# Optimization experiments

Measured on AMD Instinct MI355X. Metric: run time of the kernel, lower is better.

Reference implementation:

```python
import jax, jax.numpy as jnp
import numpy as np
from jax import lax

B, L, H, E, NIN, D = 1024, 128, 256, 256, 3, 10


def setup_inputs():
    key = jax.random.key(0)
    ks = jax.random.split(key, 32)
    s = 0.05

    def rn(i, shape):
        return jax.random.normal(ks[i], shape, dtype=jnp.float32) * s

    inp = {
        "received": jax.random.normal(ks[0], (B, L, NIN), dtype=jnp.float32),
        "encoder_hidden": jax.random.normal(ks[1], (B, L, E), dtype=jnp.float32),
        "h0": jax.random.normal(ks[2], (2, B, H), dtype=jnp.float32),
    }
    i = 3
    for r in (1, 2):
        for l, din in ((0, NIN), (1, H)):
            inp[f"w_ih{r}_l{l}"] = rn(i, (3 * H, din)); i += 1
            inp[f"w_hh{r}_l{l}"] = rn(i, (3 * H, H)); i += 1
            inp[f"b_ih{r}_l{l}"] = rn(i, (3 * H,)); i += 1
            inp[f"b_hh{r}_l{l}"] = rn(i, (3 * H,)); i += 1
    inp["attn_W"] = rn(i, (H, H + E)); i += 1
    inp["v_W"] = rn(i, (1, H)); i += 1
    inp["out_W"] = rn(i, (1, 2 * (H + E))); i += 1
    inp["out_b"] = rn(i, (1,))
    return inp


def _gru_cell(x, h, w_ih, w_hh, b_ih, b_hh):
    # PyTorch GRU cell semantics (gate order r, z, n)
    gi = x @ w_ih.T + b_ih
    gh = h @ w_hh.T + b_hh
    i_r, i_z, i_n = jnp.split(gi, 3, axis=-1)
    h_r, h_z, h_n = jnp.split(gh, 3, axis=-1)
    r = jax.nn.sigmoid(i_r + h_r)
    z = jax.nn.sigmoid(i_z + h_z)
    n = jnp.tanh(i_n + r * h_n)
    return (1.0 - z) * n + z * h


def _forward(received, encoder_hidden, h0, p1, p2, attn_W, v_W, out_W, out_b):
    # split attn weight: cat order is (s, encoder_hidden)
    W_s, W_e = attn_W[:, :H], attn_W[:, H:]
    # precompute encoder part of the attention energy once
    attn_enc = jnp.einsum('bse,he->bsh', encoder_hidden, W_e)  # [B,L,H]
    v = v_W[0]

    def attend(s_top):  # s_top: [B,H] = second-layer hidden BEFORE the RNN step
        energy = jnp.tanh((s_top @ W_s.T)[:, None, :] + attn_enc)  # [B,L,H]
        a = jax.nn.softmax(jnp.einsum('bsh,h->bs', energy, v), axis=1)
        return jnp.einsum('bs,bse->be', a, encoder_hidden)  # context [B,E]

    def rnn2(x, h, p):  # 2-layer GRU, single timestep
        h0n = _gru_cell(x, h[0], p[0], p[1], p[2], p[3])
        h1n = _gru_cell(h0n, h[1], p[4], p[5], p[6], p[7])
        return jnp.stack([h0n, h1n]), h1n

    def step(carry, x_t):
        h1, h2 = carry
        c1 = attend(h1[1])
        c2 = attend(h2[1])
        h1n, o1 = rnn2(x_t, h1, p1)
        h2n, o2 = rnn2(x_t, h2, p2)
        return (h1n, h2n), (jnp.concatenate([o1, c1], -1), jnp.concatenate([o2, c2], -1))

    xs = jnp.swapaxes(received, 0, 1)  # [L,B,NIN]
    _, (r1, r2) = lax.scan(step, (h0, h0), xs)
    rnn_out1 = jnp.swapaxes(r1, 0, 1)  # [B,L,H+E]
    rnn_out2 = jnp.swapaxes(r2, 0, 1)

    # delayed second stream: index i+D, clamped to L-1 for i >= L-D-1
    t = jnp.arange(L)
    idx = jnp.where(t >= L - D - 1, L - 1, t + D)
    rnn_out = jnp.concatenate([rnn_out1, rnn_out2[:, idx, :]], axis=-1)  # [B,L,2*(H+E)]
    return jax.nn.sigmoid(rnn_out @ out_W.T + out_b)  # [B,L,1]


def reference(received, encoder_hidden, h0,
              w_ih1_l0, w_hh1_l0, b_ih1_l0, b_hh1_l0,
              w_ih1_l1, w_hh1_l1, b_ih1_l1, b_hh1_l1,
              w_ih2_l0, w_hh2_l0, b_ih2_l0, b_hh2_l0,
              w_ih2_l1, w_hh2_l1, b_ih2_l1, b_hh2_l1,
              attn_W, v_W, out_W, out_b):
    p1 = (w_ih1_l0, w_hh1_l0, b_ih1_l0, b_hh1_l0, w_ih1_l1, w_hh1_l1, b_ih1_l1, b_hh1_l1)
    p2 = (w_ih2_l0, w_hh2_l0, b_ih2_l0, b_hh2_l0, w_ih2_l1, w_hh2_l1, b_ih2_l1, b_hh2_l1)
    return _forward(received, encoder_hidden, h0, p1, p2, attn_W, v_W, out_W, out_b)
```

## Files before the change

kernel.cpp:

```cpp
#include <hip/hip_runtime.h>

typedef unsigned int u32;
typedef unsigned short u16;
typedef __attribute__((ext_vector_type(8))) short bf8v;
typedef __attribute__((ext_vector_type(4))) float f32x4;

#define NB 1024
#define NL 128
#define NH 256

#define WS_WHH(g,l)  ((size_t)((g)*2+(l)) * 393216ull)
#define WS_WIHX(g)   (1572864ull + (size_t)(g)*49152ull)
#define WS_WIH1(g)   (1671168ull + (size_t)(g)*442368ull)
#define WS_WSPK      2555904ull
#define WS_WEPK      2686976ull
#define WS_AE        2818048ull
#define WS_HTOP      (WS_AE + 134217728ull)
#define WS_HL0       (WS_HTOP + 135266304ull)
#define WS_P         (WS_HL0 + 134217728ull)
#define WS_Q         (WS_P + 1048576ull)

struct Ins { const float* p[23]; };

__device__ __forceinline__ u16 f2b(float f) {
  u32 u = __builtin_bit_cast(u32, f);
  u += 0x7fffu + ((u >> 16) & 1u);
  return (u16)(u >> 16);
}
__device__ __forceinline__ float b2f(u16 h) { return __builtin_bit_cast(float, ((u32)h) << 16); }
__device__ __forceinline__ float upk(const uint4& q, int i) {
  u32 w = (i < 2) ? q.x : (i < 4) ? q.y : (i < 6) ? q.z : q.w;
  return (i & 1) ? __builtin_bit_cast(float, w & 0xffff0000u)
                 : __builtin_bit_cast(float, w << 16);
}
__device__ __forceinline__ float frcp(float x) { return __builtin_amdgcn_rcpf(x); }
__device__ __forceinline__ float sigm(float x)  { return frcp(1.f + __expf(-x)); }
__device__ __forceinline__ float tanh_f(float x){ return 1.f - 2.f*frcp(1.f + __expf(2.f*x)); }

__device__ __forceinline__ f32x4 MF(bf8v a, bf8v b, f32x4 c) {
  return __builtin_amdgcn_mfma_f32_16x16x32_bf16(a, b, c, 0, 0, 0);
}
__device__ __forceinline__ bf8v ld8(const u16* p) {
  return __builtin_bit_cast(bf8v, *(const uint4*)p);
}

__device__ __forceinline__ void st_h(u16* hout, const u16* hlds, int t, int b0, int tid) {
  int srow = tid >> 5, scol = (tid & 31) * 8;
  *(uint4*)(hout + ((size_t)t*NB + b0 + srow)*NH + scol) = *(const uint4*)(hlds + srow*280 + scol);
}

__global__ void k_pack(Ins in, char* ws) {
  int tile = blockIdx.x*4 + (threadIdx.x >> 6);
  int lane = threadIdx.x & 63, llo = lane & 15, lhi = lane >> 4;
  float v[8];
  u16* dst;
  if (tile < 1536) {
    int mat = tile/384, rem = tile%384, tn = rem >> 3, kt = rem & 7;
    int g = mat >> 1, l = mat & 1;
    const float* w = in.p[4 + g*8 + l*4];
    int n = tn*16 + llo;
    #pragma unroll
    for (int i = 0; i < 8; i++) { int k = kt*32 + lhi*8 + i; v[i] = w[n*256 + k]; }
    dst = (u16*)(ws + WS_WHH(g,l)) + ((size_t)(tn*8+kt)*64 + lane)*8;
  } else if (tile < 1632) {
    int t2 = tile-1536; int g = t2/48, tn = t2%48;
    const float* w  = in.p[3+g*8];
    const float* bi = in.p[5+g*8];
    const float* bh = in.p[6+g*8];
    int n = tn*16 + llo;
    #pragma unroll
    for (int i = 0; i < 8; i++) {
      int k = lhi*8 + i;
      v[i] = (k < 3) ? w[n*3+k] : (k == 3 ? (bi[n] + (n < 512 ? bh[n] : 0.f)) : 0.f);
    }
    dst = (u16*)(ws + WS_WIHX(g)) + ((size_t)tn*64 + lane)*8;
  } else if (tile < 2496) {
    int t2 = tile-1632; int g = t2/432, rem = t2%432, tn = rem/9, kt = rem%9;
    const float* w  = in.p[7+g*8];
    const float* bi = in.p[9+g*8];
    const float* bh = in.p[10+g*8];
    int n = tn*16 + llo;
    #pragma unroll
    for (int i = 0; i < 8; i++) {
      int k = kt*32 + lhi*8 + i;
      v[i] = (k < 256) ? w[n*256+k] : (k == 256 ? (bi[n] + (n < 512 ? bh[n] : 0.f)) : 0.f);
    }
    dst = (u16*)(ws + WS_WIH1(g)) + ((size_t)(tn*9+kt)*64 + lane)*8;
  } else if (tile < 2624) {
    int t2 = tile-2496, tn = t2 >> 3, kt = t2 & 7;
    const float* aw = in.p[19]; int n = tn*16 + llo;
    #pragma unroll
    for (int i = 0; i < 8; i++) { int k = kt*32 + lhi*8 + i; v[i] = aw[n*512 + k]; }
    dst = (u16*)(ws + WS_WSPK) + ((size_t)(tn*8+kt)*64 + lane)*8;
  } else {
    int t2 = tile-2624, tn = t2 >> 3, kt = t2 & 7;
    const float* aw = in.p[19]; int n = tn*16 + llo;
    #pragma unroll
    for (int i = 0; i < 8; i++) { int k = kt*32 + lhi*8 + i; v[i] = aw[n*512 + 256 + k]; }
    dst = (u16*)(ws + WS_WEPK) + ((size_t)(tn*8+kt)*64 + lane)*8;
  }
  uint4 pk;
  pk.x = (u32)f2b(v[0]) | ((u32)f2b(v[1]) << 16);
  pk.y = (u32)f2b(v[2]) | ((u32)f2b(v[3]) << 16);
  pk.z = (u32)f2b(v[4]) | ((u32)f2b(v[5]) << 16);
  pk.w = (u32)f2b(v[6]) | ((u32)f2b(v[7]) << 16);
  *(uint4*)dst = pk;
}

__global__ void k_hall0(Ins in, char* ws) {
  int idx = blockIdx.x*256 + threadIdx.x;
  int g = idx >> 18, r = idx & 262143;
  u16* ht = (u16*)(ws + WS_HTOP) + (size_t)g*(129ull*NB*NH);
  ht[r] = f2b(in.p[2][262144 + r]);
}

__global__ __launch_bounds__(512, 2) void k_attn_enc(Ins in, char* ws) {
  __shared__ __align__(16) u16 alds[128*280];
  const float* eh = in.p[1];
  const u16* wep = (const u16*)(ws + WS_WEPK);
  float* ae = (float*)(ws + WS_AE);
  float* qo = (float*)(ws + WS_Q);
  int b = blockIdx.x, tid = threadIdx.x;
  int w = tid >> 6, lane = tid & 63, llo = lane & 15, lhi = lane >> 4;
  for (int c = tid; c < 4096; c += 512) {
    int row = c >> 5, cc = c & 31;
    const float* s = eh + ((size_t)(b*128 + row))*256 + cc*8;
    float4 f0 = *(const float4*)s, f1 = *(const float4*)(s+4);
    uint4 pk;
    pk.x = (u32)f2b(f0.x) | ((u32)f2b(f0.y) << 16);
    pk.y = (u32)f2b(f0.z) | ((u32)f2b(f0.w) << 16);
    pk.z = (u32)f2b(f1.x) | ((u32)f2b(f1.y) << 16);
    pk.w = (u32)f2b(f1.z) | ((u32)f2b(f1.w) << 16);
    *(uint4*)(alds + row*280 + cc*8) = pk;
  }
  __syncthreads();
  bf8v bf[2][8];
  #pragma unroll
  for (int nt = 0; nt < 2; nt++)
    #pragma unroll
    for (int kt = 0; kt < 8; kt++)
      bf[nt][kt] = ld8(wep + (((size_t)(2*w+nt)*8 + kt)*64 + lane)*8);
  for (int mt = 0; mt < 8; mt++) {
    bf8v af[8];
    #pragma unroll
    for (int kt = 0; kt < 8; kt++)
      af[kt] = ld8(alds + (16*mt + llo)*280 + kt*32 + lhi*8);
    #pragma unroll
    for (int nt = 0; nt < 2; nt++) {
      f32x4 c = {0.f,0.f,0.f,0.f};
      #pragma unroll
      for (int kt = 0; kt < 8; kt++) c = MF(af[kt], bf[nt][kt], c);
      int h = (2*w+nt)*16 + llo;
      int s0 = 16*mt + 4*lhi;
      float4 st = { __expf(2.f*c[0]), __expf(2.f*c[1]), __expf(2.f*c[2]), __expf(2.f*c[3]) };
      *(float4*)(ae + (size_t)b*32768 + h*128 + s0) = st;
    }
  }
  if (tid < 256) {
    int qq = tid >> 7, s = tid & 127;
    const float* wc = in.p[21] + 256 + qq*512;
    float acc = 0.f;
    #pragma unroll 1
    for (int e = 0; e < 256; e += 8) {
      uint4 ev = *(const uint4*)(alds + s*280 + e);
      #pragma unroll
      for (int i = 0; i < 8; i++) acc += upk(ev, i) * wc[e + i];
    }
    qo[((size_t)qq*NB + b)*128 + s] = acc;
  }
}

__global__ __launch_bounds__(512, 2) void k_rec0(Ins in, char* ws) {
  __shared__ __align__(16) u16 hlds[16*280];
  __shared__ __align__(16) u16 xpad[16*32];
  const int g = blockIdx.y, b0 = blockIdx.x*16, tid = threadIdx.x;
  const int w = tid >> 6, lane = tid & 63, llo = lane & 15, lhi = lane >> 4;

  const u16* whh = (const u16*)(ws + WS_WHH(g,0));
  const u16* wgi = (const u16*)(ws + WS_WIHX(g));
  const float* bhh = in.p[6 + g*8];
  const float* h0  = in.p[2];
  const float* recv = in.p[0];
  u16* hout = (u16*)(ws + WS_HL0) + (size_t)g*(128ull*NB*NH);

  float bhhn[2];
  #pragma unroll
  for (int p = 0; p < 2; p++) bhhn[p] = bhh[512 + 32*w + 16*p + llo];

  bf8v whhR[2][8], whhN[2][8];
  #pragma unroll
  for (int p = 0; p < 2; p++)
    #pragma unroll
    for (int kt = 0; kt < 8; kt++) {
      whhR[p][kt] = ld8(whh + (((size_t)(      2*w + p)*8 + kt)*64 + lane)*8);
      whhN[p][kt] = ld8(whh + (((size_t)(32 + 2*w + p)*8 + kt)*64 + lane)*8);
    }

  float hst[2][4];
  #pragma unroll
  for (int r = 0; r < 4; r++) {
    int row = 4*lhi + r;
    #pragma unroll
    for (int p = 0; p < 2; p++) {
      int col = 32*w + 16*p + llo;
      float hv = h0[(size_t)(b0 + row)*NH + col];
      hst[p][r] = hv;
      hlds[row*280 + col] = f2b(hv);
    }
  }
  if (tid < 256) ((u32*)xpad)[tid] = 0u;
  __syncthreads();
  if (tid < 16) {
    const float* x = recv + (size_t)(b0 + tid)*(NL*3);
    uint2 q;
    q.x = (u32)f2b(x[0]) | ((u32)f2b(x[1]) << 16);
    q.y = (u32)f2b(x[2]) | (0x3f80u << 16);
    *(uint2*)(xpad + tid*32) = q;
  }

  #pragma unroll 1
  for (int t = 0; t < NL; t++) {
    __syncthreads();
    if (t) st_h(hout, hlds, t-1, b0, tid);
    bf8v xf = ld8(xpad + llo*32 + lhi*8);
    f32x4 aR[2], aZ[2], aNi[2], aNh[2];
    #pragma unroll
    for (int p = 0; p < 2; p++) {
      f32x4 z = {0.f,0.f,0.f,0.f};
      aR[p]=z; aZ[p]=z; aNi[p]=z; aNh[p]=z;
    }
    #pragma unroll
    for (int q = 0; q < 3; q++)
      #pragma unroll
      for (int p = 0; p < 2; p++) {
        bf8v bt = ld8(wgi + ((size_t)(16*q + 2*w + p)*64 + lane)*8);
        f32x4 a0 = (q==0) ? aR[p] : (q==1) ? aZ[p] : aNi[p];
        a0 = MF(xf, bt, a0);
        if (q==0) aR[p]=a0; else if (q==1) aZ[p]=a0; else aNi[p]=a0;
      }
    #pragma unroll
    for (int kt = 0; kt < 8; kt++) {
      bf8v hf = ld8(hlds + llo*280 + kt*32 + lhi*8);
      #pragma unroll
      for (int p = 0; p < 2; p++) {
        aR[p]  = MF(hf, whhR[p][kt], aR[p]);
        bf8v bz = ld8(whh + (((size_t)(16 + 2*w + p)*8 + kt)*64 + lane)*8);
        aZ[p]  = MF(hf, bz, aZ[p]);
        aNh[p] = MF(hf, whhN[p][kt], aNh[p]);
      }
    }
    u16 hv16[2][4];
    #pragma unroll
    for (int p = 0; p < 2; p++)
      #pragma unroll
      for (int r = 0; r < 4; r++) {
        float rr = sigm(aR[p][r]);
        float zz = sigm(aZ[p][r]);
        float nn = tanh_f(aNi[p][r] + rr*(aNh[p][r] + bhhn[p]));
        float h  = nn + zz*(hst[p][r] - nn);
        hst[p][r] = h; hv16[p][r] = f2b(h);
      }
    __syncthreads();
    #pragma unroll
    for (int r = 0; r < 4; r++) {
      int row = 4*lhi + r;
      #pragma unroll
      for (int p = 0; p < 2; p++)
        hlds[row*280 + 32*w + 16*p + llo] = hv16[p][r];
    }
    if (t < NL-1 && tid < 16) {
      const float* x = recv + (size_t)(b0 + tid)*(NL*3) + (size_t)(t+1)*3;
      uint2 q;
      q.x = (u32)f2b(x[0]) | ((u32)f2b(x[1]) << 16);
      q.y = (u32)f2b(x[2]) | (0x3f80u << 16);
      *(uint2*)(xpad + tid*32) = q;
    }
  }
  __syncthreads();
  st_h(hout, hlds, NL-1, b0, tid);
}

__global__ __launch_bounds__(512, 2) void k_rec1(Ins in, char* ws) {
  __shared__ __align__(16) u16 hlds[16*280];
  __shared__ __align__(16) u16 alds[64*296];
  __shared__ __align__(16) u32 gilds[4*768*9];
  const int g = blockIdx.y, b0 = blockIdx.x*16, tid = threadIdx.x;
  const int w = tid >> 6, lane = tid & 63, llo = lane & 15, lhi = lane >> 4;

  const u16* whh = (const u16*)(ws + WS_WHH(g,1));
  const u16* wgi = (const u16*)(ws + WS_WIH1(g));
  const float* bhh = in.p[10 + g*8];
  const float* h0  = in.p[2] + (size_t)(NB*NH);
  const u16* hl0 = (const u16*)(ws + WS_HL0) + (size_t)g*(128ull*NB*NH);
  u16* hout = (u16*)(ws + WS_HTOP) + (size_t)g*(129ull*NB*NH) + (size_t)(NB*NH);

  float bhhn[2];
  #pragma unroll
  for (int p = 0; p < 2; p++) bhhn[p] = bhh[512 + 32*w + 16*p + llo];

  bf8v whhR[2][8], whhN[2][8];
  #pragma unroll
  for (int p = 0; p < 2; p++)
    #pragma unroll
    for (int kt = 0; kt < 8; kt++) {
      whhR[p][kt] = ld8(whh + (((size_t)(      2*w + p)*8 + kt)*64 + lane)*8);
      whhN[p][kt] = ld8(whh + (((size_t)(32 + 2*w + p)*8 + kt)*64 + lane)*8);
    }

  float hst[2][4];
  #pragma unroll
  for (int r = 0; r < 4; r++) {
    int row = 4*lhi + r;
    #pragma unroll
    for (int p = 0; p < 2; p++) {
      int col = 32*w + 16*p + llo;
      float hv = h0[(size_t)(b0 + row)*NH + col];
      hst[p][r] = hv;
      hlds[row*280 + col] = f2b(hv);
    }
  }

  bf8v af8c = {0,0,0,0,0,0,0,0};
  if (lhi == 0) af8c[0] = (short)0x3f80;

  #pragma unroll 1
  for (int t = 0; t < NL; t++) {
    __syncthreads();
    if (t) st_h(hout, hlds, t-1, b0, tid);
    if ((t & 3) == 0) {
      for (int c = tid; c < 2048; c += 512) {
        int row = c >> 5, cc = c & 31;
        *(uint4*)(alds + row*296 + cc*8) =
          *(const uint4*)(hl0 + ((size_t)(t + (row>>4))*NB + b0 + (row&15))*NH + cc*8);
      }
      __syncthreads();
      #pragma unroll 1
      for (int qq = 0; qq < 3; qq++) {
        f32x4 acc[2][4];
        #pragma unroll
        for (int p = 0; p < 2; p++)
          #pragma unroll
          for (int mt = 0; mt < 4; mt++) { f32x4 z = {0.f,0.f,0.f,0.f}; acc[p][mt] = z; }
        #pragma unroll 1
        for (int kt = 0; kt < 9; kt++) {
          bf8v b0t = ld8(wgi + (((size_t)(16*qq + 2*w + 0)*9 + kt)*64 + lane)*8);
          bf8v b1t = ld8(wgi + (((size_t)(16*qq + 2*w + 1)*9 + kt)*64 + lane)*8);
          bf8v afm[4];
          #pragma unroll
          for (int mt = 0; mt < 4; mt++)
            afm[mt] = (kt < 8) ? ld8(alds + (mt*16 + llo)*296 + kt*32 + lhi*8) : af8c;
          #pragma unroll
          for (int mt = 0; mt < 4; mt++) {
            acc[0][mt] = MF(afm[mt], b0t, acc[0][mt]);
            acc[1][mt] = MF(afm[mt], b1t, acc[1][mt]);
          }
        }
        #pragma unroll
        for (int p = 0; p < 2; p++)
          #pragma unroll
          for (int mt = 0; mt < 4; mt++) {
            int col = (16*qq + 2*w + p)*16 + llo;
            u32* G = gilds + ((size_t)mt*768 + col)*9 + 2*lhi;
            G[0] = (u32)f2b(acc[p][mt][0]) | ((u32)f2b(acc[p][mt][1]) << 16);
            G[1] = (u32)f2b(acc[p][mt][2]) | ((u32)f2b(acc[p][mt][3]) << 16);
          }
      }
      __syncthreads();
    }
    f32x4 aR[2], aZ[2], aNh[2];
    float giN[2][4];
    #pragma unroll
    for (int p = 0; p < 2; p++) {
      int colb = 32*w + 16*p + llo;
      const u32* G0 = gilds + ((size_t)(t&3)*768 +       colb)*9 + 2*lhi;
      const u32* G1 = gilds + ((size_t)(t&3)*768 + 256 + colb)*9 + 2*lhi;
      const u32* G2 = gilds + ((size_t)(t&3)*768 + 512 + colb)*9 + 2*lhi;
      u32 r0 = G0[0], r1 = G0[1], z0 = G1[0], z1 = G1[1], n0 = G2[0], n1 = G2[1];
      aR[p][0] = b2f((u16)r0); aR[p][1] = b2f((u16)(r0 >> 16));
      aR[p][2] = b2f((u16)r1); aR[p][3] = b2f((u16)(r1 >> 16));
      aZ[p][0] = b2f((u16)z0); aZ[p][1] = b2f((u16)(z0 >> 16));
      aZ[p][2] = b2f((u16)z1); aZ[p][3] = b2f((u16)(z1 >> 16));
      giN[p][0] = b2f((u16)n0); giN[p][1] = b2f((u16)(n0 >> 16));
      giN[p][2] = b2f((u16)n1); giN[p][3] = b2f((u16)(n1 >> 16));
      f32x4 z = {0.f,0.f,0.f,0.f};
      aNh[p] = z;
    }
    #pragma unroll
    for (int kt = 0; kt < 8; kt++) {
      bf8v hf = ld8(hlds + llo*280 + kt*32 + lhi*8);
      #pragma unroll
      for (int p = 0; p < 2; p++) {
        aR[p]  = MF(hf, whhR[p][kt], aR[p]);
        bf8v bz = ld8(whh + (((size_t)(16 + 2*w + p)*8 + kt)*64 + lane)*8);
        aZ[p]  = MF(hf, bz, aZ[p]);
        aNh[p] = MF(hf, whhN[p][kt], aNh[p]);
      }
    }
    u16 hv16[2][4];
    #pragma unroll
    for (int p = 0; p < 2; p++)
      #pragma unroll
      for (int r = 0; r < 4; r++) {
        float rr = sigm(aR[p][r]);
        float zz = sigm(aZ[p][r]);
        float nn = tanh_f(giN[p][r] + rr*(aNh[p][r] + bhhn[p]));
        float h  = nn + zz*(hst[p][r] - nn);
        hst[p][r] = h; hv16[p][r] = f2b(h);
      }
    __syncthreads();
    #pragma unroll
    for (int r = 0; r < 4; r++) {
      int row = 4*lhi + r;
      #pragma unroll
      for (int p = 0; p < 2; p++)
        hlds[row*280 + 32*w + 16*p + llo] = hv16[p][r];
    }
  }
  __syncthreads();
  st_h(hout, hlds, NL-1, b0, tid);
}

__global__ __launch_bounds__(512, 2) void k_energy(Ins in, char* ws) {
  __shared__ __align__(16) float spE[128*66];
  __shared__ __align__(16) float aeQ[64*132];
  __shared__ __align__(16) float vE[256];
  __shared__ __align__(16) float woE[256];
  __shared__ __align__(16) float qsE[128];
  const int g = blockIdx.y, b = blockIdx.x, tid = threadIdx.x;
  const int w = tid >> 6, lane = tid & 63, llo = lane & 15, lhi = lane >> 4;
  const int gid = w*4 + lhi;
  const float* ae_g = (const float*)(ws + WS_AE) + (size_t)b*32768;
  const u16* htop = (const u16*)(ws + WS_HTOP) + (size_t)g*(129ull*NB*NH);
  const u16* wsp  = (const u16*)(ws + WS_WSPK);
  const float* qg = (const float*)(ws + WS_Q) + ((size_t)g*NB + b)*128;
  float* pw = (float*)(ws + WS_P) + (size_t)g*(NB*NL) + (size_t)b*NL;

  for (int c = tid; c < 256; c += 512) { vE[c] = in.p[20][c]; woE[c] = in.p[21][g*512 + c]; }
  if (tid < 128) qsE[tid] = qg[tid];
  __syncthreads();
  float Vtot = 0.f;
  for (int i = 0; i < 64; i++) {
    float4 v4 = *(const float4*)(vE + i*4);
    Vtot += v4.x + v4.y + v4.z + v4.w;
  }

  bf8v af[8];
  #pragma unroll
  for (int kt = 0; kt < 8; kt++)
    af[kt] = ld8(htop + ((size_t)(16*w + llo)*NB + b)*NH + kt*32 + lhi*8);

  float accS[2][2][8];
  #pragma unroll
  for (int th = 0; th < 2; th++)
    #pragma unroll
    for (int i = 0; i < 2; i++)
      #pragma unroll
      for (int s = 0; s < 8; s++) accS[th][i][s] = 0.f;

  #pragma unroll 1
  for (int hq4 = 0; hq4 < 4; hq4++) {
    __syncthreads();
    for (int c = tid; c < 2048; c += 512)
      *(float4*)(aeQ + (c>>5)*132 + (c&31)*4) =
        *(const float4*)(ae_g + (size_t)(hq4*64 + (c>>5))*128 + (c&31)*4);
    {
      #pragma unroll
      for (int nt = 0; nt < 4; nt++) {
        int tn = hq4*4 + nt;
        f32x4 c = {0.f,0.f,0.f,0.f};
        #pragma unroll
        for (int kt = 0; kt < 8; kt++) {
          bf8v bt = ld8(wsp + (((size_t)tn*8 + kt)*64 + lane)*8);
          c = MF(af[kt], bt, c);
        }
        int trow0 = 16*w + 4*lhi, hcol = nt*16 + llo;
        #pragma unroll
        for (int r = 0; r < 4; r++)
          spE[(trow0+r)*66 + hcol] = __expf(2.f*c[r]);
      }
    }
    __syncthreads();
    #pragma unroll 1
    for (int th = 0; th < 2; th++) {
      const int tl = th*64 + gid*2;
      #pragma unroll 1
      for (int hq = 0; hq < 16; hq++) {
        int h0 = hq*4;
        float4 es0 = *(const float4*)(spE + tl*66 + h0);
        float4 es1 = *(const float4*)(spE + (tl+1)*66 + h0);
        float4 vq  = *(const float4*)(vE + hq4*64 + h0);
        float ea[4][8];
        #pragma unroll
        for (int j = 0; j < 4; j++) {
          float4 eA = *(const float4*)(aeQ + (h0+j)*132 + llo*8);
          float4 eB = *(const float4*)(aeQ + (h0+j)*132 + llo*8 + 4);
          ea[j][0]=eA.x; ea[j][1]=eA.y; ea[j][2]=eA.z; ea[j][3]=eA.w;
          ea[j][4]=eB.x; ea[j][5]=eB.y; ea[j][6]=eB.z; ea[j][7]=eB.w;
        }
        #pragma unroll
        for (int s = 0; s < 8; s++) {
          {
            float D0 = fmaf(es0.x, ea[0][s], 1.f), D1 = fmaf(es0.y, ea[1][s], 1.f);
            float D2 = fmaf(es0.z, ea[2][s], 1.f), D3 = fmaf(es0.w, ea[3][s], 1.f);
            float na = fmaf(vq.y, D0, vq.x*D1), da = D0*D1;
            float nb = fmaf(vq.w, D2, vq.z*D3), db = D2*D3;
            float N = fmaf(nb, da, na*db);
            accS[th][0][s] = fmaf(N, frcp(da*db), accS[th][0][s]);
          }
          {
            float D0 = fmaf(es1.x, ea[0][s], 1.f), D1 = fmaf(es1.y, ea[1][s], 1.f);
            float D2 = fmaf(es1.z, ea[2][s], 1.f), D3 = fmaf(es1.w, ea[3][s], 1.f);
            float na = fmaf(vq.y, D0, vq.x*D1), da = D0*D1;
            float nb = fmaf(vq.w, D2, vq.z*D3), db = D2*D3;
            float N = fmaf(nb, da, na*db);
            accS[th][1][s] = fmaf(N, frcp(da*db), accS[th][1][s]);
          }
        }
      }
    }
  }
  #pragma unroll
  for (int th = 0; th < 2; th++)
    #pragma unroll
    for (int i = 0; i < 2; i++) {
      float en[8];
      #pragma unroll
      for (int s = 0; s < 8; s++) en[s] = Vtot - 2.f*accS[th][i][s];
      float mx = en[0];
      #pragma unroll
      for (int s = 1; s < 8; s++) mx = fmaxf(mx, en[s]);
      for (int d = 1; d < 16; d <<= 1) mx = fmaxf(mx, __shfl_xor(mx, d));
      float sum = 0.f, aw[8];
      #pragma unroll
      for (int s = 0; s < 8; s++) { float e = __expf(en[s] - mx); aw[s] = e; sum += e; }
      for (int d = 1; d < 16; d <<= 1) sum += __shfl_xor(sum, d);
      float dn = frcp(sum);
      int t = th*64 + gid*2 + i;
      float pv = 0.f;
      #pragma unroll
      for (int s = 0; s < 8; s++) pv += aw[s]*dn * qsE[8*llo + s];
      uint4 o0 = *(const uint4*)(htop + ((size_t)(t+1)*NB + b)*NH + 8*llo);
      uint4 o1 = *(const uint4*)(htop + ((size_t)(t+1)*NB + b)*NH + 128 + 8*llo);
      #pragma unroll
      for (int j = 0; j < 8; j++) {
        pv += upk(o0, j) * woE[8*llo + j];
        pv += upk(o1, j) * woE[128 + 8*llo + j];
      }
      for (int d = 1; d < 16; d <<= 1) pv += __shfl_xor(pv, d);
      if (llo == 0) pw[t] = pv;
    }
}

__global__ void k_final(Ins in, char* ws, float* out) {
  int idx = blockIdx.x*256 + threadIdx.x;
  int b = idx >> 7, t = idx & 127;
  const float* pw = (const float*)(ws + WS_P);
  float p1 = pw[(size_t)b*NL + t];
  int t2 = (t >= 117) ? 127 : (t + 10);
  float p2 = pw[(size_t)NB*NL + (size_t)b*NL + t2];
  out[idx] = sigm(p1 + p2 + in.p[22][0]);
}

extern "C" void kernel_launch(void* const* d_in, const int* in_sizes, int n_in,
                              void* d_out, int out_size, void* d_ws, size_t ws_size,
                              hipStream_t stream) {
  Ins in;
  for (int i = 0; i < 23; i++) in.p[i] = (const float*)d_in[i];
  char* ws = (char*)d_ws;
  k_pack    <<<688, 256, 0, stream>>>(in, ws);
  k_hall0   <<<2048, 256, 0, stream>>>(in, ws);
  k_attn_enc<<<1024, 512, 0, stream>>>(in, ws);
  k_rec0    <<<dim3(64, 2), 512, 0, stream>>>(in, ws);
  k_rec1    <<<dim3(64, 2), 512, 0, stream>>>(in, ws);
  k_energy  <<<dim3(1024, 2), 512, 0, stream>>>(in, ws);
  k_final   <<<512, 256, 0, stream>>>(in, ws, (float*)d_out);
}
```

Measured before the change: 2.247 ms.

## Split s-projection into separate kernel with fp16 exp cache and packed-FMA energy loop

Moves the s_top @ W_s projection and its exp out of k_energy into a new k_sp kernel. k_sp writes exp(2*proj), clamped and stored as fp16, into the reused HL0 workspace. The top-layer hidden-state buffer changes from time-major to batch-major, so each batch's 129 timesteps are contiguous for k_sp and k_energy. k_energy reads the fp16 cache, uses smaller LDS, raises occupancy to 4 blocks per CU, and computes the rational-tanh energy with two-wide float vectors so the compiler can emit packed FMAs. The costs are an extra kernel launch, an extra global round trip for the cache, and possible precision loss from fp16 storage and the clamp at 11.

```diff
diff --git a/kernel.cpp b/kernel.cpp
--- a/kernel.cpp
+++ b/kernel.cpp
@@ -4,6 +4,7 @@
 typedef unsigned short u16;
 typedef __attribute__((ext_vector_type(8))) short bf8v;
 typedef __attribute__((ext_vector_type(4))) float f32x4;
+typedef __attribute__((ext_vector_type(2))) float f32x2;
 
 #define NB 1024
 #define NL 128
@@ -28,6 +29,8 @@
   return (u16)(u >> 16);
 }
 __device__ __forceinline__ float b2f(u16 h) { return __builtin_bit_cast(float, ((u32)h) << 16); }
+__device__ __forceinline__ u16 f2h(float f) { _Float16 h = (_Float16)f; return __builtin_bit_cast(u16, h); }
+__device__ __forceinline__ float h2f(u16 h) { return (float)__builtin_bit_cast(_Float16, h); }
 __device__ __forceinline__ float upk(const uint4& q, int i) {
   u32 w = (i < 2) ? q.x : (i < 4) ? q.y : (i < 6) ? q.z : q.w;
   return (i & 1) ? __builtin_bit_cast(float, w & 0xffff0000u)
@@ -43,10 +46,16 @@
 __device__ __forceinline__ bf8v ld8(const u16* p) {
   return __builtin_bit_cast(bf8v, *(const uint4*)p);
 }
+__device__ __forceinline__ f32x2 lo2(const float4& v){ f32x2 r = {v.x, v.y}; return r; }
+__device__ __forceinline__ f32x2 hi2(const float4& v){ f32x2 r = {v.z, v.w}; return r; }
 
 __device__ __forceinline__ void st_h(u16* hout, const u16* hlds, int t, int b0, int tid) {
   int srow = tid >> 5, scol = (tid & 31) * 8;
   *(uint4*)(hout + ((size_t)t*NB + b0 + srow)*NH + scol) = *(const uint4*)(hlds + srow*280 + scol);
+}
+__device__ __forceinline__ void st_h2(u16* hb, const u16* hlds, int t, int b0, int tid) {
+  int srow = tid >> 5, scol = (tid & 31) * 8;
+  *(uint4*)(hb + ((size_t)(b0 + srow)*129 + (t+1))*NH + scol) = *(const uint4*)(hlds + srow*280 + scol);
 }
 
 __global__ void k_pack(Ins in, char* ws) {
@@ -110,8 +119,9 @@
 __global__ void k_hall0(Ins in, char* ws) {
   int idx = blockIdx.x*256 + threadIdx.x;
   int g = idx >> 18, r = idx & 262143;
+  int b = r >> 8, h = r & 255;
   u16* ht = (u16*)(ws + WS_HTOP) + (size_t)g*(129ull*NB*NH);
-  ht[r] = f2b(in.p[2][262144 + r]);
+  ht[((size_t)b*129)*NH + h] = f2b(in.p[2][262144 + r]);
 }
 
 __global__ __launch_bounds__(512, 2) void k_attn_enc(Ins in, char* ws) {
@@ -292,7 +302,7 @@
   const float* bhh = in.p[10 + g*8];
   const float* h0  = in.p[2] + (size_t)(NB*NH);
   const u16* hl0 = (const u16*)(ws + WS_HL0) + (size_t)g*(128ull*NB*NH);
-  u16* hout = (u16*)(ws + WS_HTOP) + (size_t)g*(129ull*NB*NH) + (size_t)(NB*NH);
+  u16* hout = (u16*)(ws + WS_HTOP) + (size_t)g*(129ull*NB*NH);
 
   float bhhn[2];
   #pragma unroll
@@ -326,7 +336,7 @@
   #pragma unroll 1
   for (int t = 0; t < NL; t++) {
     __syncthreads();
-    if (t) st_h(hout, hlds, t-1, b0, tid);
+    if (t) st_h2(hout, hlds, t-1, b0, tid);
     if ((t & 3) == 0) {
       for (int c = tid; c < 2048; c += 512) {
         int row = c >> 5, cc = c & 31;
@@ -417,12 +427,64 @@
     }
   }
   __syncthreads();
-  st_h(hout, hlds, NL-1, b0, tid);
-}
-
-__global__ __launch_bounds__(512, 2) void k_energy(Ins in, char* ws) {
-  __shared__ __align__(16) float spE[128*66];
-  __shared__ __align__(16) float aeQ[64*132];
+  st_h2(hout, hlds, NL-1, b0, tid);
+}
+
+__global__ __launch_bounds__(512, 2) void k_sp(Ins in, char* ws) {
+  __shared__ __align__(16) u16 alds[128*280];
+  const int g = blockIdx.y, b = blockIdx.x, tid = threadIdx.x;
+  const int w = tid >> 6, lane = tid & 63, llo = lane & 15, lhi = lane >> 4;
+  const u16* ht2 = (const u16*)(ws + WS_HTOP) + (size_t)g*(129ull*NB*NH) + (size_t)b*129*NH;
+  const u16* wsp = (const u16*)(ws + WS_WSPK);
+  u16* esp = (u16*)(ws + WS_HL0) + ((size_t)(g*NB + b))*32768;
+  for (int c = tid; c < 4096; c += 512) {
+    int row = c >> 5, cc = c & 31;
+    *(uint4*)(alds + row*280 + cc*8) = *(const uint4*)(ht2 + (size_t)row*NH + cc*8);
+  }
+  __syncthreads();
+  bf8v bf[2][8];
+  #pragma unroll
+  for (int nt = 0; nt < 2; nt++)
+    #pragma unroll
+    for (int kt = 0; kt < 8; kt++)
+      bf[nt][kt] = ld8(wsp + (((size_t)(2*w+nt)*8 + kt)*64 + lane)*8);
+  for (int mt = 0; mt < 8; mt++) {
+    bf8v af[8];
+    #pragma unroll
+    for (int kt = 0; kt < 8; kt++)
+      af[kt] = ld8(alds + (16*mt + llo)*280 + kt*32 + lhi*8);
+    #pragma unroll
+    for (int nt = 0; nt < 2; nt++) {
+      f32x4 c = {0.f,0.f,0.f,0.f};
+      #pragma unroll
+      for (int kt = 0; kt < 8; kt++) c = MF(af[kt], bf[nt][kt], c);
+      int h = (2*w+nt)*16 + llo, t0 = 16*mt + 4*lhi;
+      #pragma unroll
+      for (int r = 0; r < 4; r++)
+        esp[(size_t)(t0+r)*NH + h] = f2h(__expf(fminf(2.f*c[r], 11.f)));
+    }
+  }
+}
+
+__device__ __forceinline__ void quad(const float4& es, f32x2 ea0, f32x2 ea1, f32x2 ea2, f32x2 ea3,
+                                     const float4& vq, f32x2& acc) {
+  f32x2 D0 = ea0 * es.x + 1.f;
+  f32x2 D1 = ea1 * es.y + 1.f;
+  f32x2 D2 = ea2 * es.z + 1.f;
+  f32x2 D3 = ea3 * es.w + 1.f;
+  f32x2 na = D0 * vq.y + D1 * vq.x;
+  f32x2 da = D0 * D1;
+  f32x2 nb = D2 * vq.w + D3 * vq.z;
+  f32x2 db = D2 * D3;
+  f32x2 N  = na * db + nb * da;
+  f32x2 d  = da * db;
+  f32x2 r  = { frcp(d.x), frcp(d.y) };
+  acc += N * r;
+}
+
+__global__ __launch_bounds__(512, 4) void k_energy(Ins in, char* ws) {
+  __shared__ __align__(16) u16   spT[128*72];
+  __shared__ __align__(16) float aeT[64*132];
   __shared__ __align__(16) float vE[256];
   __shared__ __align__(16) float woE[256];
   __shared__ __align__(16) float qsE[128];
@@ -430,8 +492,8 @@
   const int w = tid >> 6, lane = tid & 63, llo = lane & 15, lhi = lane >> 4;
   const int gid = w*4 + lhi;
   const float* ae_g = (const float*)(ws + WS_AE) + (size_t)b*32768;
-  const u16* htop = (const u16*)(ws + WS_HTOP) + (size_t)g*(129ull*NB*NH);
-  const u16* wsp  = (const u16*)(ws + WS_WSPK);
+  const u16* esp_g  = (const u16*)(ws + WS_HL0) + ((size_t)(g*NB + b))*32768;
+  const u16* ht2b   = (const u16*)(ws + WS_HTOP) + (size_t)g*(129ull*NB*NH) + (size_t)b*129*NH;
   const float* qg = (const float*)(ws + WS_Q) + ((size_t)g*NB + b)*128;
   float* pw = (float*)(ws + WS_P) + (size_t)g*(NB*NL) + (size_t)b*NL;
 
@@ -444,78 +506,50 @@
     Vtot += v4.x + v4.y + v4.z + v4.w;
   }
 
-  bf8v af[8];
-  #pragma unroll
-  for (int kt = 0; kt < 8; kt++)
-    af[kt] = ld8(htop + ((size_t)(16*w + llo)*NB + b)*NH + kt*32 + lhi*8);
-
-  float accS[2][2][8];
+  f32x2 acc2[2][2][4];
   #pragma unroll
   for (int th = 0; th < 2; th++)
     #pragma unroll
     for (int i = 0; i < 2; i++)
       #pragma unroll
-      for (int s = 0; s < 8; s++) accS[th][i][s] = 0.f;
+      for (int p = 0; p < 4; p++) { f32x2 z = {0.f,0.f}; acc2[th][i][p] = z; }
 
   #pragma unroll 1
   for (int hq4 = 0; hq4 < 4; hq4++) {
     __syncthreads();
+    for (int c = tid; c < 1024; c += 512) {
+      int row = c >> 3, hcc = c & 7;
+      *(uint4*)(spT + row*72 + hcc*8) = *(const uint4*)(esp_g + (size_t)row*256 + hq4*64 + hcc*8);
+    }
     for (int c = tid; c < 2048; c += 512)
-      *(float4*)(aeQ + (c>>5)*132 + (c&31)*4) =
+      *(float4*)(aeT + (c>>5)*132 + (c&31)*4) =
         *(const float4*)(ae_g + (size_t)(hq4*64 + (c>>5))*128 + (c&31)*4);
-    {
-      #pragma unroll
-      for (int nt = 0; nt < 4; nt++) {
-        int tn = hq4*4 + nt;
-        f32x4 c = {0.f,0.f,0.f,0.f};
-        #pragma unroll
-        for (int kt = 0; kt < 8; kt++) {
-          bf8v bt = ld8(wsp + (((size_t)tn*8 + kt)*64 + lane)*8);
-          c = MF(af[kt], bt, c);
-        }
-        int trow0 = 16*w + 4*lhi, hcol = nt*16 + llo;
-        #pragma unroll
-        for (int r = 0; r < 4; r++)
-          spE[(trow0+r)*66 + hcol] = __expf(2.f*c[r]);
-      }
-    }
     __syncthreads();
     #pragma unroll 1
-    for (int th = 0; th < 2; th++) {
-      const int tl = th*64 + gid*2;
-      #pragma unroll 1
-      for (int hq = 0; hq < 16; hq++) {
-        int h0 = hq*4;
-        float4 es0 = *(const float4*)(spE + tl*66 + h0);
-        float4 es1 = *(const float4*)(spE + (tl+1)*66 + h0);
-        float4 vq  = *(const float4*)(vE + hq4*64 + h0);
-        float ea[4][8];
-        #pragma unroll
-        for (int j = 0; j < 4; j++) {
-          float4 eA = *(const float4*)(aeQ + (h0+j)*132 + llo*8);
-          float4 eB = *(const float4*)(aeQ + (h0+j)*132 + llo*8 + 4);
-          ea[j][0]=eA.x; ea[j][1]=eA.y; ea[j][2]=eA.z; ea[j][3]=eA.w;
-          ea[j][4]=eB.x; ea[j][5]=eB.y; ea[j][6]=eB.z; ea[j][7]=eB.w;
-        }
-        #pragma unroll
-        for (int s = 0; s < 8; s++) {
-          {
-            float D0 = fmaf(es0.x, ea[0][s], 1.f), D1 = fmaf(es0.y, ea[1][s], 1.f);
-            float D2 = fmaf(es0.z, ea[2][s], 1.f), D3 = fmaf(es0.w, ea[3][s], 1.f);
-            float na = fmaf(vq.y, D0, vq.x*D1), da = D0*D1;
-            float nb = fmaf(vq.w, D2, vq.z*D3), db = D2*D3;
-            float N = fmaf(nb, da, na*db);
-            accS[th][0][s] = fmaf(N, frcp(da*db), accS[th][0][s]);
-          }
-          {
-            float D0 = fmaf(es1.x, ea[0][s], 1.f), D1 = fmaf(es1.y, ea[1][s], 1.f);
-            float D2 = fmaf(es1.z, ea[2][s], 1.f), D3 = fmaf(es1.w, ea[3][s], 1.f);
-            float na = fmaf(vq.y, D0, vq.x*D1), da = D0*D1;
-            float nb = fmaf(vq.w, D2, vq.z*D3), db = D2*D3;
-            float N = fmaf(nb, da, na*db);
-            accS[th][1][s] = fmaf(N, frcp(da*db), accS[th][1][s]);
-          }
-        }
+    for (int hq = 0; hq < 16; hq++) {
+      int h0 = hq*4;
+      float4 eaA[4], eaB[4];
+      #pragma unroll
+      for (int j = 0; j < 4; j++) {
+        eaA[j] = *(const float4*)(aeT + (h0+j)*132 + 4*llo);
+        eaB[j] = *(const float4*)(aeT + (h0+j)*132 + 64 + 4*llo);
+      }
+      float4 vq = *(const float4*)(vE + hq4*64 + h0);
+      #pragma unroll
+      for (int th = 0; th < 2; th++) {
+        int tl = th*64 + gid*2;
+        uint2 ef0 = *(const uint2*)(spT + tl*72 + h0);
+        uint2 ef1 = *(const uint2*)(spT + (tl+1)*72 + h0);
+        float4 es0 = { h2f((u16)ef0.x), h2f((u16)(ef0.x>>16)), h2f((u16)ef0.y), h2f((u16)(ef0.y>>16)) };
+        float4 es1 = { h2f((u16)ef1.x), h2f((u16)(ef1.x>>16)), h2f((u16)ef1.y), h2f((u16)(ef1.y>>16)) };
+        quad(es0, lo2(eaA[0]), lo2(eaA[1]), lo2(eaA[2]), lo2(eaA[3]), vq, acc2[th][0][0]);
+        quad(es0, hi2(eaA[0]), hi2(eaA[1]), hi2(eaA[2]), hi2(eaA[3]), vq, acc2[th][0][1]);
+        quad(es0, lo2(eaB[0]), lo2(eaB[1]), lo2(eaB[2]), lo2(eaB[3]), vq, acc2[th][0][2]);
+        quad(es0, hi2(eaB[0]), hi2(eaB[1]), hi2(eaB[2]), hi2(eaB[3]), vq, acc2[th][0][3]);
+        quad(es1, lo2(eaA[0]), lo2(eaA[1]), lo2(eaA[2]), lo2(eaA[3]), vq, acc2[th][1][0]);
+        quad(es1, hi2(eaA[0]), hi2(eaA[1]), hi2(eaA[2]), hi2(eaA[3]), vq, acc2[th][1][1]);
+        quad(es1, lo2(eaB[0]), lo2(eaB[1]), lo2(eaB[2]), lo2(eaB[3]), vq, acc2[th][1][2]);
+        quad(es1, hi2(eaB[0]), hi2(eaB[1]), hi2(eaB[2]), hi2(eaB[3]), vq, acc2[th][1][3]);
       }
     }
   }
@@ -524,8 +558,10 @@
     #pragma unroll
     for (int i = 0; i < 2; i++) {
       float en[8];
-      #pragma unroll
-      for (int s = 0; s < 8; s++) en[s] = Vtot - 2.f*accS[th][i][s];
+      en[0] = Vtot - 2.f*acc2[th][i][0].x; en[1] = Vtot - 2.f*acc2[th][i][0].y;
+      en[2] = Vtot - 2.f*acc2[th][i][1].x; en[3] = Vtot - 2.f*acc2[th][i][1].y;
+      en[4] = Vtot - 2.f*acc2[th][i][2].x; en[5] = Vtot - 2.f*acc2[th][i][2].y;
+      en[6] = Vtot - 2.f*acc2[th][i][3].x; en[7] = Vtot - 2.f*acc2[th][i][3].y;
       float mx = en[0];
       #pragma unroll
       for (int s = 1; s < 8; s++) mx = fmaxf(mx, en[s]);
@@ -538,9 +574,11 @@
       int t = th*64 + gid*2 + i;
       float pv = 0.f;
       #pragma unroll
-      for (int s = 0; s < 8; s++) pv += aw[s]*dn * qsE[8*llo + s];
-      uint4 o0 = *(const uint4*)(htop + ((size_t)(t+1)*NB + b)*NH + 8*llo);
-      uint4 o1 = *(const uint4*)(htop + ((size_t)(t+1)*NB + b)*NH + 128 + 8*llo);
+      for (int s = 0; s < 4; s++) pv += aw[s]*dn * qsE[4*llo + s];
+      #pragma unroll
+      for (int s = 4; s < 8; s++) pv += aw[s]*dn * qsE[64 + 4*llo + (s-4)];
+      uint4 o0 = *(const uint4*)(ht2b + (size_t)(t+1)*NH + 8*llo);
+      uint4 o1 = *(const uint4*)(ht2b + (size_t)(t+1)*NH + 128 + 8*llo);
       #pragma unroll
       for (int j = 0; j < 8; j++) {
         pv += upk(o0, j) * woE[8*llo + j];
@@ -572,6 +610,7 @@
   k_attn_enc<<<1024, 512, 0, stream>>>(in, ws);
   k_rec0    <<<dim3(64, 2), 512, 0, stream>>>(in, ws);
   k_rec1    <<<dim3(64, 2), 512, 0, stream>>>(in, ws);
+  k_sp      <<<dim3(1024, 2), 512, 0, stream>>>(in, ws);
   k_energy  <<<dim3(1024, 2), 512, 0, stream>>>(in, ws);
   k_final   <<<512, 256, 0, stream>>>(in, ws, (float*)d_out);
 }
```

New measurement: 2.000 ms. -11.0%, faster.
